# Optimization experiments

Measured on AMD Instinct MI355X. Metric: run time of the kernel, lower is better.

## Reference

```python
import jax, jax.numpy as jnp
import numpy as np

N_HEADS = 16
HEAD_DIM = 64
WINDOW = 128
GLOBAL = 64


def setup_inputs() -> dict:
    key = jax.random.key(0)
    ks = jax.random.split(key, 5)
    B, T, D = 2, 8192, 1024
    s = 0.02
    return {
        "x": jax.random.normal(ks[0], (B, T, D), dtype=jnp.float32),
        "Wq": jax.random.normal(ks[1], (D, D), dtype=jnp.float32) * s,
        "Wk": jax.random.normal(ks[2], (D, D), dtype=jnp.float32) * s,
        "Wv": jax.random.normal(ks[3], (D, D), dtype=jnp.float32) * s,
        "Wo": jax.random.normal(ks[4], (D, D), dtype=jnp.float32) * s,
    }


def reference(x, Wq, Wk, Wv, Wo):
    B, T, D = x.shape
    h, hd, w = N_HEADS, HEAD_DIM, WINDOW
    g = min(GLOBAL, T)
    nw = T // w  # T chosen as a multiple of window_size
    scale = hd ** -0.5

    def proj(W):
        # nn.Linear: y = x @ W.T ; then (B,T,h,hd) -> (B,h,T,hd)
        return (x @ W.T).reshape(B, T, h, hd).transpose(0, 2, 1, 3)

    q = proj(Wq)
    k = proj(Wk)
    v = proj(Wv)

    # Chunk into non-overlapping local windows: (B,h,nw,w,hd)
    qw = q.reshape(B, h, nw, w, hd)
    kw = k.reshape(B, h, nw, w, hd)
    vw = v.reshape(B, h, nw, w, hd)
    kg = k[:, :, :g, :]  # global prefix keys (B,h,g,hd)
    vg = v[:, :, :g, :]

    # Scores against [global ++ local] keys (faithful: global prefix is
    # concatenated for every window, including windows that overlap it).
    s_g = jnp.einsum("bhnqd,bhgd->bhnqg", qw, kg) * scale  # (B,h,nw,w,g)
    s_l = jnp.einsum("bhnqd,bhnkd->bhnqk", qw, kw) * scale  # (B,h,nw,w,w)
    attn = jax.nn.softmax(jnp.concatenate([s_g, s_l], axis=-1), axis=-1)

    out = (
        jnp.einsum("bhnqg,bhgd->bhnqd", attn[..., :g], vg)
        + jnp.einsum("bhnqk,bhnkd->bhnqd", attn[..., g:], vw)
    )
    out = out.reshape(B, h, T, hd).transpose(0, 2, 1, 3).reshape(B, T, D)
    return out @ Wo.T
```

## Files before the change

### kernel.cpp

```cpp
#include <hip/hip_runtime.h>

typedef unsigned short u16;
typedef __attribute__((ext_vector_type(8))) short short8;
typedef __attribute__((ext_vector_type(4))) float f32x4;
typedef __attribute__((ext_vector_type(4))) float floatx4;
typedef __attribute__((ext_vector_type(4))) unsigned short ushort4v;
typedef __attribute__((ext_vector_type(8))) unsigned short ushort8v;

#define MFMA(a, b, c)   __builtin_amdgcn_mfma_f32_16x16x32_bf16(a, b, c, 0, 0, 0)

__device__ __forceinline__ u16 f2bf(float f) {
    unsigned u = __float_as_uint(f);
    u += 0x7fffu + ((u >> 16) & 1u);
    return (u16)(u >> 16);
}

__device__ __forceinline__ void async16(const void* g, void* l) {
    __builtin_amdgcn_global_load_lds(
        (const __attribute__((address_space(1))) void*)g,
        (__attribute__((address_space(3))) void*)l, 16, 0, 0);
}

#define PSYNC do {                                               \
    asm volatile("s_waitcnt vmcnt(6)" ::: "memory");             \
    __builtin_amdgcn_s_barrier();                                \
    asm volatile("s_waitcnt lgkmcnt(0)" ::: "memory");           \
    __builtin_amdgcn_sched_barrier(0);                           \
} while (0)

__global__ void cvt_all(const float* __restrict__ x,
                        const float* __restrict__ w0, const float* __restrict__ w1,
                        const float* __restrict__ w2, const float* __restrict__ w3,
                        u16* __restrict__ d, int nx4, int nw4) {
    int total = nx4 + 4 * nw4;
    int i = blockIdx.x * blockDim.x + threadIdx.x;
    int stride = gridDim.x * blockDim.x;
    for (; i < total; i += stride) {
        floatx4 v;
        if (i < nx4) {
            v = ((const floatx4*)x)[i];
        } else {
            int t = i - nx4;
            int w = t >> 18;
            int j = t & (nw4 - 1);
            const float* s = w == 0 ? w0 : (w == 1 ? w1 : (w == 2 ? w2 : w3));
            v = ((const floatx4*)s)[j];
        }
        ushort4v o;
        o[0] = f2bf(v[0]); o[1] = f2bf(v[1]); o[2] = f2bf(v[2]); o[3] = f2bf(v[3]);
        ((ushort4v*)d)[i] = o;
    }
}

template <bool BF16_OUT>
__global__ __launch_bounds__(512, 2) void gemm_nt(
    const u16* __restrict__ A, const u16* __restrict__ B0,
    const u16* __restrict__ B1, const u16* __restrict__ B2,
    void* __restrict__ Cv, int M, int N, int K)
{
    __shared__ u16 As[2][16384];
    __shared__ u16 Bs[2][16384];
    const int tid = threadIdx.x;
    const int wave = tid >> 6, lane = tid & 63;
    const int tl = lane & 15, quad = lane >> 4, xr = lane & 7;
    const int wm = wave >> 2, wn = wave & 3;
    const int m0 = blockIdx.x * 256, n0 = blockIdx.y * 256;
    const u16* Bm = blockIdx.z == 0 ? B0 : (blockIdx.z == 1 ? B1 : B2);
    const size_t coff = (size_t)blockIdx.z * M * N;

    f32x4 acc[8][4];
#pragma unroll
    for (int i = 0; i < 8; i++)
#pragma unroll
        for (int j = 0; j < 4; j++) acc[i][j] = (f32x4)(0.0f);

    const int rw = lane >> 3, sl = lane & 7;
    const int g = sl ^ rw;
    const u16* a_srcb = A  + (size_t)(m0 + wave * 8 + rw) * K + g * 8;
    const u16* b_srcb = Bm + (size_t)(n0 + wm * 64 + wn * 8 + rw) * K + g * 8;
    u16* asd = &As[0][0] + wave * 512;
    u16* bsd = &Bs[0][0] + wm * 4096 + wn * 512;

#define STG_A(t, h, p) do {                                                              \
    async16(a_srcb + (size_t)((h) * 64) * K + (size_t)(t) * 64,                          \
            asd + (p) * 16384 + (h) * 4096);                                             \
    async16(a_srcb + (size_t)((h) * 64 + 128) * K + (size_t)(t) * 64,                    \
            asd + (p) * 16384 + (h) * 4096 + 8192);                                      \
} while (0)
#define STG_B(t, h, p) do {                                                              \
    async16(b_srcb + (size_t)((h) * 32) * K + (size_t)(t) * 64,                          \
            bsd + (p) * 16384 + (h) * 2048);                                             \
    async16(b_srcb + (size_t)((h) * 32 + 128) * K + (size_t)(t) * 64,                    \
            bsd + (p) * 16384 + (h) * 2048 + 8192);                                      \
} while (0)

    const int NT = K >> 6;
    const u16* Ab0 = &As[0][0] + (wm * 128 + tl) * 64;
    const u16* Bb0 = &Bs[0][0] + (wn * 64 + tl) * 64;
    const int s0 = (quad ^ xr) * 8;

    short8 afA[4][2], afB[4][2], bfA[2][2], bfB[2][2];

    STG_A(0, 0, 0); STG_B(0, 0, 0); STG_A(0, 1, 0); STG_B(0, 1, 0);
    STG_A(1, 0, 1); STG_B(1, 0, 1);
    asm volatile("s_waitcnt vmcnt(8)" ::: "memory");
    __builtin_amdgcn_s_barrier();
    __builtin_amdgcn_sched_barrier(0);

    for (int t = 0; t < NT; ++t) {
        const int p = t & 1;
        const int t1 = (t + 1 < NT) ? t + 1 : NT - 1;
        const int t2 = (t + 2 < NT) ? t + 2 : NT - 1;
        const int b1 = (t + 1) & 1, b2 = t & 1;
        const u16* Ab = Ab0 + p * 16384;
        const u16* Bb = Bb0 + p * 16384;

#pragma unroll
        for (int i = 0; i < 4; i++) {
            afA[i][0] = *(const short8*)(Ab + i * 1024 + s0);
            afA[i][1] = *(const short8*)(Ab + i * 1024 + (s0 ^ 32));
        }
#pragma unroll
        for (int j = 0; j < 2; j++) {
            bfA[j][0] = *(const short8*)(Bb + j * 1024 + s0);
            bfA[j][1] = *(const short8*)(Bb + j * 1024 + (s0 ^ 32));
        }
        STG_A(t1, 1, b1);
        PSYNC;
        __builtin_amdgcn_s_setprio(1);
#pragma unroll
        for (int kh = 0; kh < 2; kh++)
#pragma unroll
            for (int i = 0; i < 4; i++)
#pragma unroll
                for (int j = 0; j < 2; j++)
                    acc[i][j] = MFMA(afA[i][kh], bfA[j][kh], acc[i][j]);
        __builtin_amdgcn_s_setprio(0);
        __builtin_amdgcn_s_barrier();

#pragma unroll
        for (int i = 0; i < 4; i++) {
            afB[i][0] = *(const short8*)(Ab + (4 + i) * 1024 + s0);
            afB[i][1] = *(const short8*)(Ab + (4 + i) * 1024 + (s0 ^ 32));
        }
        STG_B(t1, 1, b1);
        PSYNC;
        __builtin_amdgcn_s_setprio(1);
#pragma unroll
        for (int kh = 0; kh < 2; kh++)
#pragma unroll
            for (int i = 0; i < 4; i++)
#pragma unroll
                for (int j = 0; j < 2; j++)
                    acc[4 + i][j] = MFMA(afB[i][kh], bfA[j][kh], acc[4 + i][j]);
        __builtin_amdgcn_s_setprio(0);
        __builtin_amdgcn_s_barrier();

#pragma unroll
        for (int j = 0; j < 2; j++) {
            bfB[j][0] = *(const short8*)(Bb + (2 + j) * 1024 + s0);
            bfB[j][1] = *(const short8*)(Bb + (2 + j) * 1024 + (s0 ^ 32));
        }
        STG_A(t2, 0, b2);
        PSYNC;
        __builtin_amdgcn_s_setprio(1);
#pragma unroll
        for (int kh = 0; kh < 2; kh++)
#pragma unroll
            for (int i = 0; i < 4; i++)
#pragma unroll
                for (int j = 0; j < 2; j++)
                    acc[4 + i][2 + j] = MFMA(afB[i][kh], bfB[j][kh], acc[4 + i][2 + j]);
        __builtin_amdgcn_s_setprio(0);
        __builtin_amdgcn_s_barrier();

        STG_B(t2, 0, b2);
        PSYNC;
        __builtin_amdgcn_s_setprio(1);
#pragma unroll
        for (int kh = 0; kh < 2; kh++)
#pragma unroll
            for (int i = 0; i < 4; i++)
#pragma unroll
                for (int j = 0; j < 2; j++)
                    acc[i][2 + j] = MFMA(afA[i][kh], bfB[j][kh], acc[i][2 + j]);
        __builtin_amdgcn_s_setprio(0);
        __builtin_amdgcn_s_barrier();
    }
#undef STG_A
#undef STG_B
    asm volatile("s_waitcnt vmcnt(0)" ::: "memory");

#pragma unroll
    for (int mf = 0; mf < 8; mf++)
#pragma unroll
        for (int nf = 0; nf < 4; nf++)
#pragma unroll
            for (int r = 0; r < 4; r++) {
                int row = m0 + wm * 128 + mf * 16 + quad * 4 + r;
                int col = n0 + wn * 64 + nf * 16 + tl;
                if constexpr (BF16_OUT)
                    ((u16*)Cv)[coff + (size_t)row * N + col] = f2bf(acc[mf][nf][r]);
                else
                    ((float*)Cv)[coff + (size_t)row * N + col] = acc[mf][nf][r];
            }
}

__global__ __launch_bounds__(512) void attn_win(
    const u16* __restrict__ qkv, u16* __restrict__ outb)
{
    constexpr int T = 8192, D = 1024, HD = 64, G = 64, WIN = 128;
    constexpr int MTOT = 2 * T;
    __shared__ u16 Vs[192 * 64];
    __shared__ u16 Ks[192 * 64];
    __shared__ u16 Vt[64 * 200];

    const int blk = blockIdx.x;
    const int nwin = blk & 63;
    const int h = (blk >> 6) & 15;
    const int b = blk >> 10;
    const int tid = threadIdx.x;
    const int wave = tid >> 6, lane = tid & 63;
    const int quad = lane >> 4, tl = lane & 15;
    const int win0 = nwin * WIN;
    const size_t brow = (size_t)b * T;
    const u16* qb = qkv;
    const u16* kb = qkv + (size_t)MTOT * D;
    const u16* vb = qkv + (size_t)2 * MTOT * D;

    short8 bq[2];
    {
        int tok = win0 + wave * 16 + tl;
        const u16* qrow = qb + (brow + tok) * D + h * HD;
        bq[0] = *(const short8*)(qrow + quad * 8);
        bq[1] = *(const short8*)(qrow + 32 + quad * 8);
    }
    __builtin_amdgcn_sched_barrier(0);

#pragma unroll
    for (int i = 0; i < 3; i++) {
        int ch = i * 512 + tid;
        int row = ch >> 3, c = ch & 7;
        int tok = row < G ? row : win0 + (row - G);
        async16(vb + (brow + tok) * D + h * HD + c * 8,
                Vs + (i * 512 + wave * 64) * 8);
    }
#pragma unroll
    for (int i = 0; i < 3; i++) {
        int ch = i * 512 + tid;
        int row = ch >> 3, slot = ch & 7;
        int gg = slot ^ (row & 7);
        int tok = row < G ? row : win0 + (row - G);
        async16(kb + (brow + tok) * D + h * HD + gg * 8,
                Ks + (i * 512 + wave * 64) * 8);
    }

    asm volatile("s_waitcnt vmcnt(3)" ::: "memory");
    __builtin_amdgcn_s_barrier();
    __builtin_amdgcn_sched_barrier(0);

    {
        const int d = lane;
#pragma unroll
        for (int i = 0; i < 3; i++) {
            int c = wave * 3 + i;
            ushort8v v;
#pragma unroll
            for (int j = 0; j < 8; j++) v[j] = Vs[(c * 8 + j) * 64 + d];
            *(ushort8v*)&Vt[d * 200 + c * 8] = v;
        }
    }

    asm volatile("s_waitcnt vmcnt(0) lgkmcnt(0)" ::: "memory");
    __builtin_amdgcn_s_barrier();
    __builtin_amdgcn_sched_barrier(0);

    f32x4 s[12];
#pragma unroll
    for (int kt = 0; kt < 12; kt++) s[kt] = (f32x4)(0.0f);
#pragma unroll
    for (int kt = 0; kt < 12; kt++) {
        int row = kt * 16 + tl;
        int sa = quad ^ (tl & 7);
        int sb = (4 + quad) ^ (tl & 7);
        short8 a0 = *(const short8*)&Ks[row * 64 + sa * 8];
        short8 a1 = *(const short8*)&Ks[row * 64 + sb * 8];
        s[kt] = MFMA(a0, bq[0], s[kt]);
        s[kt] = MFMA(a1, bq[1], s[kt]);
    }

    const float c1 = 0.125f * 1.4426950408889634f;
    float mx = -1e30f;
#pragma unroll
    for (int kt = 0; kt < 12; kt++)
#pragma unroll
        for (int r = 0; r < 4; r++) mx = fmaxf(mx, s[kt][r]);
    mx = fmaxf(mx, __shfl_xor(mx, 16, 64));
    mx = fmaxf(mx, __shfl_xor(mx, 32, 64));
    float sum = 0.f;
#pragma unroll
    for (int kt = 0; kt < 12; kt++)
#pragma unroll
        for (int r = 0; r < 4; r++) {
            float e = exp2f((s[kt][r] - mx) * c1);
            s[kt][r] = e;
            sum += e;
        }
    sum += __shfl_xor(sum, 16, 64);
    sum += __shfl_xor(sum, 32, 64);
    float inv = 1.f / sum;

    __syncthreads();

    const int lq = wave * 16 + tl;
    u16* Pr = (lq < 64) ? (Vs + lq * 192) : (Ks + (lq - 64) * 192);
#pragma unroll
    for (int kt = 0; kt < 12; kt++) {
        ushort4v pk;
#pragma unroll
        for (int r = 0; r < 4; r++) pk[r] = f2bf(s[kt][r] * inv);
        *(ushort4v*)&Pr[((((kt * 2) + (quad >> 1)) ^ (lq & 7)) << 3) + ((quad & 1) << 2)] = pk;
    }
    __syncthreads();

    f32x4 o[4];
#pragma unroll
    for (int dt = 0; dt < 4; dt++) o[dt] = (f32x4)(0.0f);
#pragma unroll
    for (int ks = 0; ks < 6; ks++) {
        short8 pa = *(const short8*)&Pr[(((ks * 4) + quad) ^ (lq & 7)) << 3];
#pragma unroll
        for (int dt = 0; dt < 4; dt++) {
            short8 vv = *(const short8*)&Vt[(dt * 16 + tl) * 200 + ks * 32 + quad * 8];
            o[dt] = MFMA(pa, vv, o[dt]);
        }
    }

#pragma unroll
    for (int dt = 0; dt < 4; dt++)
#pragma unroll
        for (int r = 0; r < 4; r++) {
            int qq = win0 + wave * 16 + quad * 4 + r;
            int dim = dt * 16 + tl;
            outb[(brow + qq) * D + h * HD + dim] = f2bf(o[dt][r]);
        }
}

extern "C" void kernel_launch(void* const* d_in, const int* in_sizes, int n_in,
                              void* d_out, int out_size, void* d_ws, size_t ws_size,
                              hipStream_t stream)
{
    const float* x  = (const float*)d_in[0];
    const float* Wq = (const float*)d_in[1];
    const float* Wk = (const float*)d_in[2];
    const float* Wv = (const float*)d_in[3];
    const float* Wo = (const float*)d_in[4];

    const int M = 16384, D = 1024;
    u16* xb  = (u16*)d_ws;
    u16* wqb = xb  + (size_t)M * D;
    u16* wob = wqb + (size_t)3 * D * D;
    u16* qkv = wob + (size_t)D * D;
    u16* att = qkv + (size_t)3 * M * D;

    cvt_all<<<2560, 256, 0, stream>>>(x, Wq, Wk, Wv, Wo, xb,
                                      M * D / 4, D * D / 4);

    gemm_nt<true ><<<dim3(M / 256, D / 256, 3), 512, 0, stream>>>(
        xb, wqb, wqb + (size_t)D * D, wqb + (size_t)2 * D * D, qkv, M, D, D);
    attn_win<<<dim3(2048), 512, 0, stream>>>(qkv, att);
    gemm_nt<false><<<dim3(M / 256, D / 256, 1), 512, 0, stream>>>(
        att, wob, wob, wob, d_out, M, D, D);
}
```

Baseline: 320.9 us.

## Restructure GEMM pipeline to one-tile prefetch with fewer barriers; set attn occupancy hint

The bf16 GEMM main loop now prefetches only the next K tile into the other LDS buffer, using four staged async loads instead of staging two tiles ahead. It waits on vmcnt at three points per iteration instead of four synchronisations plus extra barriers, and it drops the explicit lgkmcnt wait. The goal is less barrier and wait overhead per iteration, at the cost of a shorter prefetch distance and possible LDS read/write hazards now that the trailing barriers are gone. The attention kernel also gets a launch_bounds minimum of 4 blocks per CU, which may force register limits.

New measurement: 303.9 us, median of 3. 5.3% less time.

```diff
diff --git a/kernel.cpp b/kernel.cpp
--- a/kernel.cpp
+++ b/kernel.cpp
@@ -21,10 +21,10 @@
         (__attribute__((address_space(3))) void*)l, 16, 0, 0);
 }
 
-#define PSYNC do {                                               \
-    asm volatile("s_waitcnt vmcnt(6)" ::: "memory");             \
+#define SYNC(n) do {                                             \
+    asm volatile("s_waitcnt vmcnt(" #n ")" ::: "memory");        \
     __builtin_amdgcn_s_barrier();                                \
-    asm volatile("s_waitcnt lgkmcnt(0)" ::: "memory");           \
+    asm volatile("" ::: "memory");                               \
     __builtin_amdgcn_sched_barrier(0);                           \
 } while (0)
 
@@ -77,9 +77,9 @@
     const int rw = lane >> 3, sl = lane & 7;
     const int g = sl ^ rw;
     const u16* a_srcb = A  + (size_t)(m0 + wave * 8 + rw) * K + g * 8;
-    const u16* b_srcb = Bm + (size_t)(n0 + wm * 64 + wn * 8 + rw) * K + g * 8;
+    const u16* b_srcb = Bm + (size_t)(n0 + (wave >> 2) * 64 + (wave & 3) * 8 + rw) * K + g * 8;
     u16* asd = &As[0][0] + wave * 512;
-    u16* bsd = &Bs[0][0] + wm * 4096 + wn * 512;
+    u16* bsd = &Bs[0][0] + (wave >> 2) * 4096 + (wave & 3) * 512;
 
 #define STG_A(t, h, p) do {                                                              \
     async16(a_srcb + (size_t)((h) * 64) * K + (size_t)(t) * 64,                          \
@@ -102,19 +102,14 @@
     short8 afA[4][2], afB[4][2], bfA[2][2], bfB[2][2];
 
     STG_A(0, 0, 0); STG_B(0, 0, 0); STG_A(0, 1, 0); STG_B(0, 1, 0);
-    STG_A(1, 0, 1); STG_B(1, 0, 1);
-    asm volatile("s_waitcnt vmcnt(8)" ::: "memory");
-    __builtin_amdgcn_s_barrier();
-    __builtin_amdgcn_sched_barrier(0);
 
     for (int t = 0; t < NT; ++t) {
-        const int p = t & 1;
-        const int t1 = (t + 1 < NT) ? t + 1 : NT - 1;
-        const int t2 = (t + 2 < NT) ? t + 2 : NT - 1;
-        const int b1 = (t + 1) & 1, b2 = t & 1;
+        const int p = t & 1, pq = p ^ 1;
+        const bool pf = (t + 1) < NT;
         const u16* Ab = Ab0 + p * 16384;
         const u16* Bb = Bb0 + p * 16384;
 
+        SYNC(4);
 #pragma unroll
         for (int i = 0; i < 4; i++) {
             afA[i][0] = *(const short8*)(Ab + i * 1024 + s0);
@@ -125,8 +120,7 @@
             bfA[j][0] = *(const short8*)(Bb + j * 1024 + s0);
             bfA[j][1] = *(const short8*)(Bb + j * 1024 + (s0 ^ 32));
         }
-        STG_A(t1, 1, b1);
-        PSYNC;
+        if (pf) STG_A(t + 1, 0, pq);
         __builtin_amdgcn_s_setprio(1);
 #pragma unroll
         for (int kh = 0; kh < 2; kh++)
@@ -136,15 +130,14 @@
                 for (int j = 0; j < 2; j++)
                     acc[i][j] = MFMA(afA[i][kh], bfA[j][kh], acc[i][j]);
         __builtin_amdgcn_s_setprio(0);
-        __builtin_amdgcn_s_barrier();
-
+
+        if (pf) { SYNC(4); } else { SYNC(2); }
 #pragma unroll
         for (int i = 0; i < 4; i++) {
             afB[i][0] = *(const short8*)(Ab + (4 + i) * 1024 + s0);
             afB[i][1] = *(const short8*)(Ab + (4 + i) * 1024 + (s0 ^ 32));
         }
-        STG_B(t1, 1, b1);
-        PSYNC;
+        if (pf) STG_B(t + 1, 0, pq);
         __builtin_amdgcn_s_setprio(1);
 #pragma unroll
         for (int kh = 0; kh < 2; kh++)
@@ -154,15 +147,14 @@
                 for (int j = 0; j < 2; j++)
                     acc[4 + i][j] = MFMA(afB[i][kh], bfA[j][kh], acc[4 + i][j]);
         __builtin_amdgcn_s_setprio(0);
-        __builtin_amdgcn_s_barrier();
-
+
+        if (pf) { SYNC(4); } else { SYNC(0); }
 #pragma unroll
         for (int j = 0; j < 2; j++) {
             bfB[j][0] = *(const short8*)(Bb + (2 + j) * 1024 + s0);
             bfB[j][1] = *(const short8*)(Bb + (2 + j) * 1024 + (s0 ^ 32));
         }
-        STG_A(t2, 0, b2);
-        PSYNC;
+        if (pf) STG_A(t + 1, 1, pq);
         __builtin_amdgcn_s_setprio(1);
 #pragma unroll
         for (int kh = 0; kh < 2; kh++)
@@ -172,10 +164,8 @@
                 for (int j = 0; j < 2; j++)
                     acc[4 + i][2 + j] = MFMA(afB[i][kh], bfB[j][kh], acc[4 + i][2 + j]);
         __builtin_amdgcn_s_setprio(0);
-        __builtin_amdgcn_s_barrier();
-
-        STG_B(t2, 0, b2);
-        PSYNC;
+
+        if (pf) STG_B(t + 1, 1, pq);
         __builtin_amdgcn_s_setprio(1);
 #pragma unroll
         for (int kh = 0; kh < 2; kh++)
@@ -185,11 +175,9 @@
                 for (int j = 0; j < 2; j++)
                     acc[i][2 + j] = MFMA(afA[i][kh], bfB[j][kh], acc[i][2 + j]);
         __builtin_amdgcn_s_setprio(0);
-        __builtin_amdgcn_s_barrier();
     }
 #undef STG_A
 #undef STG_B
-    asm volatile("s_waitcnt vmcnt(0)" ::: "memory");
 
 #pragma unroll
     for (int mf = 0; mf < 8; mf++)
@@ -206,7 +194,7 @@
             }
 }
 
-__global__ __launch_bounds__(512) void attn_win(
+__global__ __launch_bounds__(512, 4) void attn_win(
     const u16* __restrict__ qkv, u16* __restrict__ outb)
 {
     constexpr int T = 8192, D = 1024, HD = 64, G = 64, WIN = 128;
```
